# Kernel tuning notes

Hardware: AMD Instinct MI355X
Metric: run time of the kernel (lower is better)

The kernel has to match this reference:

```python
import jax, jax.numpy as jnp
import numpy as np

# Static problem dims (match input_specs / init_kwargs)
B, NQ, C, H = 2, 900, 256, 8
HGT, WID = 64, 64            # single-scale feature map (input_spatial_shapes = [[64, 64]])
N = HGT * WID                # 4096 keys
DH = C // H                  # head dim 32
RPE_HID = 512
STRIDE = 16                  # feature_stride


def setup_inputs() -> dict:
    key = jax.random.key(0)
    ks = jax.random.split(key, 24)
    p = lambda k, shape: jax.random.normal(k, shape, jnp.float32) * 0.02
    # reference boxes (cx, cy, w, h) in pixel coords of a 1024x1024 image
    ref = jax.random.uniform(ks[0], (B, NQ, 1, 4), jnp.float32)
    ref = jnp.concatenate([ref[..., :2] * (WID * STRIDE), ref[..., 2:] * 128.0], axis=-1)
    return {
        "vggt_features": jnp.zeros((1,), jnp.float32),  # unused by forward (kept for signature fidelity)
        "query": jax.random.normal(ks[1], (B, NQ, C), jnp.float32),
        "reference_2d": ref,
        "k_input_flatten": jax.random.normal(ks[2], (B, N, C), jnp.float32),
        "v_input_flatten": jax.random.normal(ks[3], (B, N, C), jnp.float32),
        "input_spatial_shapes": jnp.array([[HGT, WID]], jnp.int32),
        "input_padding_mask": jnp.zeros((B, N), jnp.bool_),
        # cpb_mlp1 (x) and cpb_mlp2 (y): Linear(2,512)+ReLU+Linear(512,H,no bias); stored as [in,out]
        "W1x": p(ks[4], (2, RPE_HID)), "b1x": jnp.zeros((RPE_HID,), jnp.float32), "W2x": p(ks[5], (RPE_HID, H)),
        "W1y": p(ks[6], (2, RPE_HID)), "b1y": jnp.zeros((RPE_HID,), jnp.float32), "W2y": p(ks[7], (RPE_HID, H)),
        "Wq": p(ks[8], (C, C)), "bq": jnp.zeros((C,), jnp.float32),
        "Wk": p(ks[9], (C, C)), "bk": jnp.zeros((C,), jnp.float32),
        "Wv": p(ks[10], (C, C)), "bv": jnp.zeros((C,), jnp.float32),
        "Wp": p(ks[11], (C, C)), "bp": jnp.zeros((C,), jnp.float32),
    }


def _mlp(d, W1, b1, W2):
    return jax.nn.relu(d @ W1 + b1) @ W2


def reference(vggt_features, query, reference_2d, k_input_flatten, v_input_flatten,
              input_spatial_shapes, input_padding_mask,
              W1x, b1x, W2x, W1y, b1y, W2y, Wq, bq, Wk, bk, Wv, bv, Wp, bp):
    h, w = HGT, WID  # static (input_spatial_shapes[0] == [HGT, WID])
    scale = DH ** -0.5
    # cxcywh -> xyxy: [B, NQ, 1, 4]
    xyxy = jnp.concatenate([reference_2d[..., :2] - reference_2d[..., 2:] / 2,
                            reference_2d[..., :2] + reference_2d[..., 2:] / 2], axis=-1)
    # pixel-center grid coords (linspace(0.5, w-0.5, w) * stride)
    pos_x = ((jnp.arange(w, dtype=jnp.float32) + 0.5) * STRIDE)[None, None, :, None]
    pos_y = ((jnp.arange(h, dtype=jnp.float32) + 0.5) * STRIDE)[None, None, :, None]
    delta_x = xyxy[..., 0::2] - pos_x  # [B, NQ, w, 2]  (x1, x2 rel. to columns)
    delta_y = xyxy[..., 1::2] - pos_y  # [B, NQ, h, 2]  (y1, y2 rel. to rows)
    rpe_x = _mlp(delta_x, W1x, b1x, W2x)  # [B, NQ, w, H]
    rpe_y = _mlp(delta_y, W1y, b1y, W2y)  # [B, NQ, h, H]
    # broadcast add over (row, col) then flatten spatial -> [B, H, NQ, N]
    rpe = (rpe_x[:, :, None] + rpe_y[:, :, :, None]).reshape(B, NQ, h * w, H).transpose(0, 3, 1, 2)
    q = (query @ Wq + bq).reshape(B, NQ, H, DH).transpose(0, 2, 1, 3) * scale  # [B,H,NQ,DH]
    k = (k_input_flatten @ Wk + bk).reshape(B, N, H, DH).transpose(0, 2, 1, 3)  # [B,H,N,DH]
    v = (v_input_flatten @ Wv + bv).reshape(B, N, H, DH).transpose(0, 2, 1, 3)  # [B,H,N,DH]
    attn = jnp.einsum('bhqd,bhkd->bhqk', q, k) + rpe
    attn = attn + input_padding_mask[:, None, None, :].astype(attn.dtype) * (-100.0)
    # torch.clip_ to finfo(min,max) is an identity on finite values; softmax follows
    attn = jax.nn.softmax(attn, axis=-1)
    x = jnp.einsum('bhqk,bhkd->bhqd', attn, v).transpose(0, 2, 1, 3).reshape(B, NQ, C)
    return x @ Wp + bp
```

## Files before the change

kernel.cpp:

```cpp
#include <hip/hip_runtime.h>
#include <hip/hip_bf16.h>
#include <cmath>

#define B_ 2
#define NQ_ 900
#define N_ 4096
#define LOG2E 1.4426950408889634f

typedef __attribute__((ext_vector_type(4))) float f32x4;
typedef __attribute__((ext_vector_type(8))) short s16x8;
typedef __attribute__((ext_vector_type(8))) _Float16 f16x8;

__device__ inline short f2bf(float x) {
    union { __hip_bfloat16 b; short s; } u;
    u.b = __float2bfloat16(x);
    return u.s;
}
__device__ inline short f2h(float x) {
    _Float16 h = (_Float16)x;
    return __builtin_bit_cast(short, h);
}

template <int CTRL>
__device__ inline float dppf(float x) {
    int xi = __builtin_bit_cast(int, x);
    int r = __builtin_amdgcn_update_dpp(xi, xi, CTRL, 0xF, 0xF, true);
    return __builtin_bit_cast(float, r);
}
__device__ inline float rowmax16(float v) {
    v = fmaxf(v, dppf<0x121>(v));
    v = fmaxf(v, dppf<0x122>(v));
    v = fmaxf(v, dppf<0x124>(v));
    v = fmaxf(v, dppf<0x128>(v));
    return v;
}
__device__ inline float rowsum16(float v) {
    v += dppf<0x121>(v);
    v += dppf<0x122>(v);
    v += dppf<0x124>(v);
    v += dppf<0x128>(v);
    return v;
}

__global__ __launch_bounds__(256) void proj_kernel(
    const float* __restrict__ query, const float* __restrict__ kin,
    const float* __restrict__ vin,
    const float* __restrict__ Wq, const float* __restrict__ Wk,
    const float* __restrict__ Wv,
    const float* __restrict__ bqv, const float* __restrict__ bkv,
    const float* __restrict__ bvv,
    unsigned short* __restrict__ qbf, unsigned short* __restrict__ kbf,
    unsigned short* __restrict__ vbf, float qscale)
{
    const int mtx = blockIdx.z;
    const float* X = mtx == 0 ? query : mtx == 1 ? kin : vin;
    const float* W = mtx == 0 ? Wq : mtx == 1 ? Wk : Wv;
    const float* bias = mtx == 0 ? bqv : mtx == 1 ? bkv : bvv;
    unsigned short* Y = mtx == 0 ? qbf : mtx == 1 ? kbf : vbf;
    const int M = mtx == 0 ? 1800 : 8192;
    const int m0 = blockIdx.x * 64;
    if (m0 >= M) return;
    const float alpha = mtx == 0 ? qscale : 1.0f;
    const int rows_per_b = mtx == 0 ? 900 : 4096;
    const int ROWS = mtx == 0 ? 960 : 4096;

    __shared__ short Ab[16384];
    __shared__ short Bb[16384];
    const int tid = threadIdx.x;
    const int w = tid >> 6, l = tid & 63, quad = l >> 4, l15 = l & 15;
    const int wq = tid & 3, mm = tid >> 2;

    {
        const bool valid = (m0 + mm) < M;
        const float* xr = X + (size_t)(m0 + mm) * 256;
        #pragma unroll
        for (int it = 0; it < 8; ++it) {
            int g2 = it * 4 + wq;
            float4 a0 = make_float4(0.f, 0.f, 0.f, 0.f), a1 = a0;
            if (valid) {
                a0 = *(const float4*)(xr + g2 * 8);
                a1 = *(const float4*)(xr + g2 * 8 + 4);
            }
            uint4 pk;
            pk.x = (unsigned)(unsigned short)f2bf(a0.x) | ((unsigned)(unsigned short)f2bf(a0.y) << 16);
            pk.y = (unsigned)(unsigned short)f2bf(a0.z) | ((unsigned)(unsigned short)f2bf(a0.w) << 16);
            pk.z = (unsigned)(unsigned short)f2bf(a1.x) | ((unsigned)(unsigned short)f2bf(a1.y) << 16);
            pk.w = (unsigned)(unsigned short)f2bf(a1.z) | ((unsigned)(unsigned short)f2bf(a1.w) << 16);
            *(uint4*)(Ab + (it * 256 + mm * 4 + wq) * 8) = pk;
        }
    }

    for (int nt0 = 0; nt0 < 4; ++nt0) {
        const int n0 = nt0 * 64;
        {
            const float* wcol = W + n0 + mm;
            #pragma unroll
            for (int it = 0; it < 8; ++it) {
                int g2 = it * 4 + wq;
                uint4 wk4;
                wk4.x = (unsigned)(unsigned short)f2bf(wcol[(g2 * 8 + 0) * 256])
                      | ((unsigned)(unsigned short)f2bf(wcol[(g2 * 8 + 1) * 256]) << 16);
                wk4.y = (unsigned)(unsigned short)f2bf(wcol[(g2 * 8 + 2) * 256])
                      | ((unsigned)(unsigned short)f2bf(wcol[(g2 * 8 + 3) * 256]) << 16);
                wk4.z = (unsigned)(unsigned short)f2bf(wcol[(g2 * 8 + 4) * 256])
                      | ((unsigned)(unsigned short)f2bf(wcol[(g2 * 8 + 5) * 256]) << 16);
                wk4.w = (unsigned)(unsigned short)f2bf(wcol[(g2 * 8 + 6) * 256])
                      | ((unsigned)(unsigned short)f2bf(wcol[(g2 * 8 + 7) * 256]) << 16);
                *(uint4*)(Bb + (it * 256 + mm * 4 + wq) * 8) = wk4;
            }
        }
        __syncthreads();

        f32x4 acc[4] = {{0.f,0.f,0.f,0.f},{0.f,0.f,0.f,0.f},{0.f,0.f,0.f,0.f},{0.f,0.f,0.f,0.f}};
        #pragma unroll
        for (int kc = 0; kc < 8; ++kc) {
            s16x8 a = *(const s16x8*)(Ab + (kc * 256 + (w * 16 + l15) * 4 + quad) * 8);
            #pragma unroll
            for (int nt = 0; nt < 4; ++nt) {
                s16x8 bf = *(const s16x8*)(Bb + (kc * 256 + (nt * 16 + l15) * 4 + quad) * 8);
                acc[nt] = __builtin_amdgcn_mfma_f32_16x16x32_bf16(a, bf, acc[nt], 0, 0, 0);
            }
        }
        __syncthreads();

        #pragma unroll
        for (int nt = 0; nt < 4; ++nt) {
            int n = n0 + nt * 16 + l15;
            float bs = bias[n];
            int h = n >> 5, d = n & 31;
            #pragma unroll
            for (int r = 0; r < 4; ++r) {
                int row = m0 + w * 16 + quad * 4 + r;
                if (row < M) {
                    int b = row / rows_per_b;
                    int pos = row - b * rows_per_b;
                    Y[((size_t)(b * 8 + h) * ROWS + pos) * 32 + d] =
                        (unsigned short)f2bf((acc[nt][r] + bs) * alpha);
                }
            }
        }
    }
}

__global__ __launch_bounds__(256) void outproj_kernel(
    const float* __restrict__ X, const float* __restrict__ W,
    const float* __restrict__ bias, float* __restrict__ Y, int M)
{
    __shared__ short Abh[4096], Abl[4096], Bbh[4096], Bbl[4096];
    const int tid = threadIdx.x;
    const int m0 = blockIdx.x * 64, n0 = blockIdx.y * 64;
    const int w = tid >> 6, l = tid & 63, quad = l >> 4, l15 = l & 15;
    const int wq = tid & 3, mm = tid >> 2;
    const bool valid = (m0 + mm) < M;
    const float* xr = X + (size_t)(m0 + mm) * 256;
    const float* wcol = W + n0 + mm;

    f32x4 acc[4] = {{0.f,0.f,0.f,0.f},{0.f,0.f,0.f,0.f},{0.f,0.f,0.f,0.f},{0.f,0.f,0.f,0.f}};

    for (int kq = 0; kq < 4; ++kq) {
        #pragma unroll
        for (int it = 0; it < 2; ++it) {
            int g2 = it * 4 + wq;
            int kbase = kq * 64 + g2 * 8;
            float av[8], bv[8];
            #pragma unroll
            for (int j = 0; j < 8; ++j) {
                av[j] = valid ? xr[kbase + j] : 0.f;
                bv[j] = wcol[(kbase + j) * 256];
            }
            uint4 ah, al, bh, bl;
            unsigned* ahp = (unsigned*)&ah; unsigned* alp = (unsigned*)&al;
            unsigned* bhp = (unsigned*)&bh; unsigned* blp = (unsigned*)&bl;
            #pragma unroll
            for (int j2 = 0; j2 < 4; ++j2) {
                _Float16 h0 = (_Float16)av[j2 * 2], h1 = (_Float16)av[j2 * 2 + 1];
                ahp[j2] = (unsigned)(unsigned short)__builtin_bit_cast(short, h0)
                        | ((unsigned)(unsigned short)__builtin_bit_cast(short, h1) << 16);
                alp[j2] = (unsigned)(unsigned short)f2h(av[j2 * 2] - (float)h0)
                        | ((unsigned)(unsigned short)f2h(av[j2 * 2 + 1] - (float)h1) << 16);
                _Float16 g0 = (_Float16)bv[j2 * 2], g1 = (_Float16)bv[j2 * 2 + 1];
                bhp[j2] = (unsigned)(unsigned short)__builtin_bit_cast(short, g0)
                        | ((unsigned)(unsigned short)__builtin_bit_cast(short, g1) << 16);
                blp[j2] = (unsigned)(unsigned short)f2h(bv[j2 * 2] - (float)g0)
                        | ((unsigned)(unsigned short)f2h(bv[j2 * 2 + 1] - (float)g1) << 16);
            }
            int gi = (it * 256 + mm * 4 + wq) * 8;
            *(uint4*)(Abh + gi) = ah;
            *(uint4*)(Abl + gi) = al;
            *(uint4*)(Bbh + gi) = bh;
            *(uint4*)(Bbl + gi) = bl;
        }
        __syncthreads();

        #pragma unroll
        for (int kc = 0; kc < 2; ++kc) {
            int ga = (kc * 256 + (w * 16 + l15) * 4 + quad) * 8;
            f16x8 ah = *(const f16x8*)(Abh + ga);
            f16x8 al = *(const f16x8*)(Abl + ga);
            #pragma unroll
            for (int nt = 0; nt < 4; ++nt) {
                int gb = (kc * 256 + (nt * 16 + l15) * 4 + quad) * 8;
                f16x8 bh = *(const f16x8*)(Bbh + gb);
                f16x8 bl = *(const f16x8*)(Bbl + gb);
                acc[nt] = __builtin_amdgcn_mfma_f32_16x16x32_f16(ah, bh, acc[nt], 0, 0, 0);
                acc[nt] = __builtin_amdgcn_mfma_f32_16x16x32_f16(ah, bl, acc[nt], 0, 0, 0);
                acc[nt] = __builtin_amdgcn_mfma_f32_16x16x32_f16(al, bh, acc[nt], 0, 0, 0);
            }
        }
        __syncthreads();
    }

    #pragma unroll
    for (int nt = 0; nt < 4; ++nt) {
        int n = n0 + nt * 16 + l15;
        float bs = bias[n];
        #pragma unroll
        for (int r = 0; r < 4; ++r) {
            int row = m0 + w * 16 + quad * 4 + r;
            if (row < M)
                Y[(size_t)row * 256 + n] = acc[nt][r] + bs;
        }
    }
}

__global__ __launch_bounds__(512) void rpe3_kernel(
    const float* __restrict__ ref2d,
    const float* __restrict__ W1x, const float* __restrict__ b1x,
    const float* __restrict__ W1y, const float* __restrict__ b1y,
    const float* __restrict__ W2x, const float* __restrict__ W2y,
    float* __restrict__ rpe_x, float* __restrict__ rpe_y)
{
    __shared__ short sw2h[8192], sw2l[8192];
    __shared__ float4 sUV[2 * 576];

    const int tid = threadIdx.x;
    for (int i = tid; i < 8192; i += 512) {
        int g = i >> 3, j = i & 7;
        int kcg = g >> 6, rr = g & 63, n = rr >> 2, q4 = rr & 3;
        int k = kcg * 32 + q4 * 8 + j;
        float val = ((n < 8) ? W2x[k * 8 + n] : W2y[k * 8 + (n - 8)]) * LOG2E;
        _Float16 hi = (_Float16)val;
        sw2h[i] = __builtin_bit_cast(short, hi);
        sw2l[i] = f2h(val - (float)hi);
    }
    {
        int k = tid;
        float w1x0 = W1x[k], w1x1 = W1x[512 + k];
        float w1y0 = W1y[k], w1y1 = W1y[512 + k];
        float bx = b1x[k], by = b1y[k];
        float vx = -(w1x0 + w1x1), vy = -(w1y0 + w1y1);
        #pragma unroll
        for (int q2 = 0; q2 < 2; ++q2) {
            const float4 bb = *(const float4*)(ref2d + (size_t)(blockIdx.x * 2 + q2) * 4);
            float ux = fmaf(w1x0, bb.x - bb.z * 0.5f, fmaf(w1x1, bb.x + bb.z * 0.5f, bx));
            float uy = fmaf(w1y0, bb.y - bb.w * 0.5f, fmaf(w1y1, bb.y + bb.w * 0.5f, by));
            sUV[q2 * 576 + (k >> 3) * 9 + (k & 7)] = make_float4(ux, vx, uy, vy);
        }
    }

    const int w = tid >> 6, l = tid & 63, quad = l >> 4, l15 = l & 15;
    const int qi = w >> 2, wrow = w & 3;
    const int bq = blockIdx.x * 2 + qi;
    const int row = wrow * 16 + l15;
    const float pc = (row + 0.5f) * 16.0f;

    __syncthreads();

    f32x4 accx = {0.f, 0.f, 0.f, 0.f}, accy = {0.f, 0.f, 0.f, 0.f};
    for (int kc = 0; kc < 16; ++kc) {
        f16x8 axh, axl, ayh, ayl;
        #pragma unroll
        for (int i = 0; i < 8; ++i) {
            float4 u = sUV[qi * 576 + (kc * 4 + quad) * 9 + i];
            float hx = fmaxf(fmaf(u.y, pc, u.x), 0.f);
            float hy = fmaxf(fmaf(u.w, pc, u.z), 0.f);
            _Float16 xh = (_Float16)hx;
            _Float16 yh = (_Float16)hy;
            axh[i] = xh;
            axl[i] = (_Float16)(hx - (float)xh);
            ayh[i] = yh;
            ayl[i] = (_Float16)(hy - (float)yh);
        }
        f16x8 bh = *(const f16x8*)(sw2h + (kc * 64 + l15 * 4 + quad) * 8);
        f16x8 bl = *(const f16x8*)(sw2l + (kc * 64 + l15 * 4 + quad) * 8);
        accx = __builtin_amdgcn_mfma_f32_16x16x32_f16(axh, bh, accx, 0, 0, 0);
        accx = __builtin_amdgcn_mfma_f32_16x16x32_f16(axh, bl, accx, 0, 0, 0);
        accx = __builtin_amdgcn_mfma_f32_16x16x32_f16(axl, bh, accx, 0, 0, 0);
        accy = __builtin_amdgcn_mfma_f32_16x16x32_f16(ayh, bh, accy, 0, 0, 0);
        accy = __builtin_amdgcn_mfma_f32_16x16x32_f16(ayh, bl, accy, 0, 0, 0);
        accy = __builtin_amdgcn_mfma_f32_16x16x32_f16(ayl, bh, accy, 0, 0, 0);
    }

    #pragma unroll
    for (int rr = 0; rr < 4; ++rr) {
        int row_out = wrow * 16 + quad * 4 + rr;
        if (l15 < 8) rpe_x[((size_t)l15 * 1800 + bq) * 64 + row_out] = accx[rr];
        else         rpe_y[((size_t)(l15 - 8) * 1800 + bq) * 64 + row_out] = accy[rr];
    }
}

__global__ __launch_bounds__(512, 4) void attn_mfma_kernel(
    const unsigned short* __restrict__ qb16, const unsigned short* __restrict__ kb16,
    const unsigned short* __restrict__ vb16,
    const float* __restrict__ rpe_x, const float* __restrict__ rpe_y,
    const unsigned char* __restrict__ mask, float* __restrict__ part)
{
    __shared__ short skf[4 * 2048];
    __shared__ short svt[4 * 2048];
    __shared__ short spb[8 * 544];
    __shared__ float sry[32 * 33];
    __shared__ unsigned long long smaskb[32];
    __shared__ float sm[8][16], sl[8][16], sMf[32], sLf[32];

    const int tid = threadIdx.x;
    const int qb = blockIdx.x, b = blockIdx.z;
    const int h = blockIdx.y & 7, kv = blockIdx.y >> 3;
    const int q0 = qb * 32;
    const int w = tid >> 6, l = tid & 63;
    const int qsub = w >> 3 ? 0 : 0;
    const int qs = w >> 2, g = w & 3;
    const int quad = l >> 4, l15 = l & 15;

    const unsigned short* qg = qb16 + (size_t)(b * 8 + h) * 960 * 32;
    const unsigned short* kg = kb16 + (size_t)(b * 8 + h) * 4096 * 32 + (size_t)kv * 2048 * 32;
    const unsigned short* vg = vb16 + (size_t)(b * 8 + h) * 4096 * 32 + (size_t)kv * 2048 * 32;
    const float* rxh = rpe_x + ((size_t)h * 1800 + b * NQ_) * 64;
    const float* ryh = rpe_y + ((size_t)h * 1800 + b * NQ_) * 64;

    for (int i = tid; i < 1024; i += 512) {
        int qq = q0 + (i >> 5), p = i & 31;
        float vy = 0.f;
        if (qq < NQ_)
            vy = ryh[(size_t)qq * 64 + kv * 32 + p];
        sry[(i >> 5) * 33 + p] = vy;
    }
    #pragma unroll
    for (int j = 0; j < 4; ++j) {
        int c = w * 4 + j;
        unsigned long long bits = __ballot(mask[(size_t)b * N_ + (kv * 32 + c) * 64 + l] != 0);
        if (l == 0) smaskb[c] = bits;
    }

    s16x8 qa = *(const s16x8*)(qg + (size_t)(q0 + qs * 16 + l15) * 32 + quad * 8);

    f32x4 rx4[4];
    #pragma unroll
    for (int t = 0; t < 4; ++t)
        #pragma unroll
        for (int r = 0; r < 4; ++r) {
            int qq = q0 + qs * 16 + quad * 4 + r;
            rx4[t][r] = (qq < NQ_) ? rxh[(size_t)qq * 64 + t * 16 + l15] : 0.f;
        }

    const int sg = tid >> 7, role = (tid >> 6) & 1, stl = tid & 63;
    int eoff[4];
    if (role == 0) {
        #pragma unroll
        for (int t = 0; t < 4; ++t)
            eoff[t] = (t * 16 + (stl & 15)) * 32 + (stl >> 4) * 8;
    } else {
        #pragma unroll
        for (int t = 0; t < 4; ++t)
            eoff[t] = stl * 32 + t * 8;
    }
    const unsigned short* src = role ? vg : kg;

    uint4 pf[4];
    {
        size_t cb = (size_t)(sg * 8) * 2048;
        #pragma unroll
        for (int t = 0; t < 4; ++t) pf[t] = *(const uint4*)(src + cb + eoff[t]);
    }

    float mrow[4] = {-INFINITY, -INFINITY, -INFINITY, -INFINITY};
    float lrow[4] = {0.f, 0.f, 0.f, 0.f};
    f32x4 acc0 = {0.f, 0.f, 0.f, 0.f}, acc1 = {0.f, 0.f, 0.f, 0.f};
    short* pw = spb + w * 544;

    for (int i = 0; i < 8; ++i) {
        __syncthreads();
        if (role == 0) {
            #pragma unroll
            for (int t = 0; t < 4; ++t)
                *(uint4*)(skf + sg * 2048 + (t * 64 + stl) * 8) = pf[t];
        } else {
            short* vtw = svt + sg * 2048;
            #pragma unroll
            for (int t = 0; t < 4; ++t) {
                const unsigned short* pv = (const unsigned short*)&pf[t];
                #pragma unroll
                for (int j = 0; j < 8; ++j) {
                    int d = t * 8 + j;
                    vtw[d * 64 + (((stl >> 3) ^ (d & 7)) << 3) + (stl & 7)] = (short)pv[j];
                }
            }
        }
        __syncthreads();

        {
            int inext = (i + 1 < 8) ? i + 1 : 7;
            size_t cb = (size_t)(sg * 8 + inext) * 2048;
            #pragma unroll
            for (int t = 0; t < 4; ++t) pf[t] = *(const uint4*)(src + cb + eoff[t]);
        }

        const int lc = g * 8 + i;
        const short* kf = skf + g * 2048;

        f32x4 sc[4];
        #pragma unroll
        for (int t = 0; t < 4; ++t) {
            s16x8 kb = *(const s16x8*)(kf + (t * 64 + l) * 8);
            sc[t] = __builtin_amdgcn_mfma_f32_16x16x32_bf16(qa, kb, rx4[t], 0, 0, 0);
        }
        float ryv[4];
        #pragma unroll
        for (int r = 0; r < 4; ++r)
            ryv[r] = sry[(qs * 16 + quad * 4 + r) * 33 + lc];
        unsigned long long mb = smaskb[lc];
        if (mb) {
            #pragma unroll
            for (int t = 0; t < 4; ++t) {
                float mk = ((mb >> (t * 16 + l15)) & 1ULL) ? -144.2695f : 0.f;
                #pragma unroll
                for (int r = 0; r < 4; ++r) sc[t][r] += mk;
            }
        }

        float cmr[4];
        #pragma unroll
        for (int r = 0; r < 4; ++r)
            cmr[r] = fmaxf(fmaxf(sc[0][r], sc[1][r]), fmaxf(sc[2][r], sc[3][r])) + ryv[r];

        int ok = (cmr[0] <= mrow[0] + 8.f) & (cmr[1] <= mrow[1] + 8.f)
               & (cmr[2] <= mrow[2] + 8.f) & (cmr[3] <= mrow[3] + 8.f);
        if (!__all(ok)) {
            #pragma unroll
            for (int r = 0; r < 4; ++r) {
                float cm = rowmax16(cmr[r]);
                float mnew = fmaxf(mrow[r], cm);
                float al = exp2f(mrow[r] - mnew);
                mrow[r] = mnew;
                lrow[r] *= al;
                acc0[r] *= al;
                acc1[r] *= al;
            }
        }

        float msub[4];
        #pragma unroll
        for (int r = 0; r < 4; ++r) msub[r] = mrow[r] - ryv[r];
        #pragma unroll
        for (int t = 0; t < 4; ++t)
            #pragma unroll
            for (int r = 0; r < 4; ++r)
                sc[t][r] = exp2f(sc[t][r] - msub[r]);
        #pragma unroll
        for (int r = 0; r < 4; ++r)
            lrow[r] += (sc[0][r] + sc[1][r]) + (sc[2][r] + sc[3][r]);

        const short* vt = svt + g * 2048;
        #pragma unroll
        for (int hh = 0; hh < 2; ++hh) {
            #pragma unroll
            for (int tt = 0; tt < 2; ++tt) {
                int t = hh * 2 + tt;
                int gphys = (tt * 2 + (l15 >> 3)) ^ quad;
                #pragma unroll
                for (int r = 0; r < 4; ++r)
                    pw[(gphys * 17 + quad * 4 + r) * 8 + (l15 & 7)] = f2bf(sc[t][r]);
            }
            int gph_r = quad ^ (l15 >> 2);
            s16x8 pa  = *(const s16x8*)(pw + (gph_r * 17 + l15) * 8);
            int ksw = ((hh * 4 + quad) ^ (l15 & 7)) * 8;
            s16x8 vb0 = *(const s16x8*)(vt + l15 * 64 + ksw);
            s16x8 vb1 = *(const s16x8*)(vt + (16 + l15) * 64 + ksw);
            acc0 = __builtin_amdgcn_mfma_f32_16x16x32_bf16(pa, vb0, acc0, 0, 0, 0);
            acc1 = __builtin_amdgcn_mfma_f32_16x16x32_bf16(pa, vb1, acc1, 0, 0, 0);
        }
    }

    #pragma unroll
    for (int r = 0; r < 4; ++r) lrow[r] = rowsum16(lrow[r]);

    __syncthreads();
    if (l15 == 0) {
        #pragma unroll
        for (int r = 0; r < 4; ++r) {
            sm[w][quad * 4 + r] = mrow[r];
            sl[w][quad * 4 + r] = lrow[r];
        }
    }
    __syncthreads();
    float wgt[4], L4[4], M4[4];
    #pragma unroll
    for (int r = 0; r < 4; ++r) {
        int qrow = quad * 4 + r;
        float mm = -INFINITY;
        #pragma unroll
        for (int gg = 0; gg < 4; ++gg) mm = fmaxf(mm, sm[qs * 4 + gg][qrow]);
        float LL = 0.f;
        #pragma unroll
        for (int gg = 0; gg < 4; ++gg)
            LL += exp2f(sm[qs * 4 + gg][qrow] - mm) * sl[qs * 4 + gg][qrow];
        wgt[r] = exp2f(mrow[r] - mm);
        L4[r] = LL;
        M4[r] = mm;
    }
    if (g == 0 && l15 == 0) {
        #pragma unroll
        for (int r = 0; r < 4; ++r) {
            sLf[qs * 16 + quad * 4 + r] = L4[r];
            sMf[qs * 16 + quad * 4 + r] = M4[r];
        }
    }

    float* obuf = (float*)skf;
    for (int gg = 0; gg < 4; ++gg) {
        if (g == gg) {
            #pragma unroll
            for (int r = 0; r < 4; ++r) {
                int idx = (qs * 16 + quad * 4 + r) * 33 + l15;
                float v0 = wgt[r] * acc0[r];
                float v1 = wgt[r] * acc1[r];
                if (gg == 0) { obuf[idx] = v0; obuf[idx + 16] = v1; }
                else         { obuf[idx] += v0; obuf[idx + 16] += v1; }
            }
        }
        __syncthreads();
    }

    float* po = part + (size_t)(((b * 8 + h) * 29 + qb) * 2 + kv) * 1088;
    for (int i = tid; i < 1024; i += 512)
        po[i] = obuf[(i >> 5) * 33 + (i & 31)];
    if (tid < 32) {
        po[1024 + tid] = sMf[tid];
        po[1056 + tid] = sLf[tid];
    }
}

__global__ __launch_bounds__(256) void attn_merge_kernel(
    const float* __restrict__ part, float* __restrict__ xout)
{
    const int qb = blockIdx.x, h = blockIdx.y, b = blockIdx.z;
    const float* p0 = part + (size_t)(((b * 8 + h) * 29 + qb) * 2) * 1088;
    const float* p1 = p0 + 1088;
    __shared__ float a0s[32], a1s[32], iLs[32];
    const int tid = threadIdx.x;
    if (tid < 32) {
        float m0 = p0[1024 + tid], m1 = p1[1024 + tid];
        float M = fmaxf(m0, m1);
        float a0 = exp2f(m0 - M), a1 = exp2f(m1 - M);
        float L = a0 * p0[1056 + tid] + a1 * p1[1056 + tid];
        a0s[tid] = a0; a1s[tid] = a1; iLs[tid] = 1.0f / L;
    }
    __syncthreads();
    int i = tid * 4;
    int ql = i >> 5, d = i & 31;
    int qq = qb * 32 + ql;
    if (qq < NQ_) {
        const f32x4 v0 = *(const f32x4*)(p0 + i);
        const f32x4 v1 = *(const f32x4*)(p1 + i);
        float a0 = a0s[ql], a1 = a1s[ql], iL = iLs[ql];
        f32x4 o;
        #pragma unroll
        for (int j = 0; j < 4; ++j)
            o[j] = (a0 * v0[j] + a1 * v1[j]) * iL;
        *(f32x4*)(&xout[(size_t)(b * NQ_ + qq) * 256 + h * 32 + d]) = o;
    }
}

extern "C" void kernel_launch(void* const* d_in, const int* in_sizes, int n_in,
                              void* d_out, int out_size, void* d_ws, size_t ws_size,
                              hipStream_t stream)
{
    const float* query = (const float*)d_in[1];
    const float* ref2d = (const float*)d_in[2];
    const float* kin   = (const float*)d_in[3];
    const float* vin   = (const float*)d_in[4];
    const unsigned char* mask = (const unsigned char*)d_in[6];
    const float* W1x = (const float*)d_in[7];
    const float* b1x = (const float*)d_in[8];
    const float* W2x = (const float*)d_in[9];
    const float* W1y = (const float*)d_in[10];
    const float* b1y = (const float*)d_in[11];
    const float* W2y = (const float*)d_in[12];
    const float* Wq  = (const float*)d_in[13];
    const float* bq  = (const float*)d_in[14];
    const float* Wk  = (const float*)d_in[15];
    const float* bk  = (const float*)d_in[16];
    const float* Wv  = (const float*)d_in[17];
    const float* bv  = (const float*)d_in[18];
    const float* Wp  = (const float*)d_in[19];
    const float* bp  = (const float*)d_in[20];

    char* wsb = (char*)d_ws;
    unsigned short* qbf = (unsigned short*)(wsb);
    unsigned short* kbf = (unsigned short*)(wsb +   983040);
    unsigned short* vbf = (unsigned short*)(wsb +  5177344);
    float* rxws = (float*)(wsb +  9371648);
    float* ryws = (float*)(wsb + 13058048);
    float* xws  = (float*)(wsb + 16744448);
    float* part = (float*)(wsb + 18587648);
    float* out  = (float*)d_out;

    const float qscale = LOG2E / sqrtf(32.0f);

    proj_kernel<<<dim3(128, 1, 3), 256, 0, stream>>>(
        query, kin, vin, Wq, Wk, Wv, bq, bk, bv, qbf, kbf, vbf, qscale);
    rpe3_kernel<<<900, 512, 0, stream>>>(
        ref2d, W1x, b1x, W1y, b1y, W2x, W2y, rxws, ryws);
    attn_mfma_kernel<<<dim3(29, 16, B_), 512, 0, stream>>>(
        qbf, kbf, vbf, rxws, ryws, mask, part);
    attn_merge_kernel<<<dim3(29, 8, B_), 256, 0, stream>>>(part, xws);
    outproj_kernel<<<dim3(29, 4), 256, 0, stream>>>(xws, Wp, bp, out, 1800);
}
```

Measured before the change: 235.0 us.

## Transpose QK MFMA so P stays in registers and feeds PV directly

Swaps the MFMA operand order for QK^T so each lane holds one query row's scores, which makes the row max and row sum lane-local (only cross-quad shuffles are needed) and removes the per-row DPP reductions. The P matrix is converted with packed fp16 and fed straight into 16x16x16 f16 MFMAs from registers, removing the shared-memory round trip through spb. V is now stored as fp16 to match. The launch-bounds occupancy hint rises to 8, which puts pressure on register allocation. The change also trades bf16 for fp16 precision on P and V.

```diff
diff --git a/kernel.cpp b/kernel.cpp
--- a/kernel.cpp
+++ b/kernel.cpp
@@ -10,6 +10,8 @@
 typedef __attribute__((ext_vector_type(4))) float f32x4;
 typedef __attribute__((ext_vector_type(8))) short s16x8;
 typedef __attribute__((ext_vector_type(8))) _Float16 f16x8;
+typedef __attribute__((ext_vector_type(4))) __fp16 h16x4;
+typedef __attribute__((ext_vector_type(2))) __fp16 h16x2;
 
 __device__ inline short f2bf(float x) {
     union { __hip_bfloat16 b; short s; } u;
@@ -19,27 +21,6 @@
 __device__ inline short f2h(float x) {
     _Float16 h = (_Float16)x;
     return __builtin_bit_cast(short, h);
-}
-
-template <int CTRL>
-__device__ inline float dppf(float x) {
-    int xi = __builtin_bit_cast(int, x);
-    int r = __builtin_amdgcn_update_dpp(xi, xi, CTRL, 0xF, 0xF, true);
-    return __builtin_bit_cast(float, r);
-}
-__device__ inline float rowmax16(float v) {
-    v = fmaxf(v, dppf<0x121>(v));
-    v = fmaxf(v, dppf<0x122>(v));
-    v = fmaxf(v, dppf<0x124>(v));
-    v = fmaxf(v, dppf<0x128>(v));
-    return v;
-}
-__device__ inline float rowsum16(float v) {
-    v += dppf<0x121>(v);
-    v += dppf<0x122>(v);
-    v += dppf<0x124>(v);
-    v += dppf<0x128>(v);
-    return v;
 }
 
 __global__ __launch_bounds__(256) void proj_kernel(
@@ -134,8 +115,9 @@
                 if (row < M) {
                     int b = row / rows_per_b;
                     int pos = row - b * rows_per_b;
+                    float v = (acc[nt][r] + bs) * alpha;
                     Y[((size_t)(b * 8 + h) * ROWS + pos) * 32 + d] =
-                        (unsigned short)f2bf((acc[nt][r] + bs) * alpha);
+                        (unsigned short)(mtx == 2 ? f2h(v) : f2bf(v));
                 }
             }
         }
@@ -299,7 +281,7 @@
     }
 }
 
-__global__ __launch_bounds__(512, 4) void attn_mfma_kernel(
+__global__ __launch_bounds__(512, 8) void attn_mfma_kernel(
     const unsigned short* __restrict__ qb16, const unsigned short* __restrict__ kb16,
     const unsigned short* __restrict__ vb16,
     const float* __restrict__ rpe_x, const float* __restrict__ rpe_y,
@@ -307,7 +289,6 @@
 {
     __shared__ short skf[4 * 2048];
     __shared__ short svt[4 * 2048];
-    __shared__ short spb[8 * 544];
     __shared__ float sry[32 * 33];
     __shared__ unsigned long long smaskb[32];
     __shared__ float sm[8][16], sl[8][16], sMf[32], sLf[32];
@@ -317,7 +298,6 @@
     const int h = blockIdx.y & 7, kv = blockIdx.y >> 3;
     const int q0 = qb * 32;
     const int w = tid >> 6, l = tid & 63;
-    const int qsub = w >> 3 ? 0 : 0;
     const int qs = w >> 2, g = w & 3;
     const int quad = l >> 4, l15 = l & 15;
 
@@ -328,11 +308,10 @@
     const float* ryh = rpe_y + ((size_t)h * 1800 + b * NQ_) * 64;
 
     for (int i = tid; i < 1024; i += 512) {
-        int qq = q0 + (i >> 5), p = i & 31;
-        float vy = 0.f;
-        if (qq < NQ_)
-            vy = ryh[(size_t)qq * 64 + kv * 32 + p];
-        sry[(i >> 5) * 33 + p] = vy;
+        int p = i & 31, ql = i >> 5;
+        int qq = q0 + ql;
+        float vy = (qq < NQ_) ? ryh[(size_t)qq * 64 + kv * 32 + p] : 0.f;
+        sry[p * 33 + ql] = vy;
     }
     #pragma unroll
     for (int j = 0; j < 4; ++j) {
@@ -343,14 +322,13 @@
 
     s16x8 qa = *(const s16x8*)(qg + (size_t)(q0 + qs * 16 + l15) * 32 + quad * 8);
 
+    const int qq_l = q0 + qs * 16 + l15;
     f32x4 rx4[4];
     #pragma unroll
     for (int t = 0; t < 4; ++t)
         #pragma unroll
-        for (int r = 0; r < 4; ++r) {
-            int qq = q0 + qs * 16 + quad * 4 + r;
-            rx4[t][r] = (qq < NQ_) ? rxh[(size_t)qq * 64 + t * 16 + l15] : 0.f;
-        }
+        for (int r = 0; r < 4; ++r)
+            rx4[t][r] = (qq_l < NQ_) ? rxh[(size_t)qq_l * 64 + t * 16 + quad * 4 + r] : 0.f;
 
     const int sg = tid >> 7, role = (tid >> 6) & 1, stl = tid & 63;
     int eoff[4];
@@ -372,10 +350,9 @@
         for (int t = 0; t < 4; ++t) pf[t] = *(const uint4*)(src + cb + eoff[t]);
     }
 
-    float mrow[4] = {-INFINITY, -INFINITY, -INFINITY, -INFINITY};
-    float lrow[4] = {0.f, 0.f, 0.f, 0.f};
+    float mrow = -INFINITY;
+    float lrow = 0.f;
     f32x4 acc0 = {0.f, 0.f, 0.f, 0.f}, acc1 = {0.f, 0.f, 0.f, 0.f};
-    short* pw = spb + w * 544;
 
     for (int i = 0; i < 8; ++i) {
         __syncthreads();
@@ -411,108 +388,83 @@
         #pragma unroll
         for (int t = 0; t < 4; ++t) {
             s16x8 kb = *(const s16x8*)(kf + (t * 64 + l) * 8);
-            sc[t] = __builtin_amdgcn_mfma_f32_16x16x32_bf16(qa, kb, rx4[t], 0, 0, 0);
-        }
-        float ryv[4];
-        #pragma unroll
-        for (int r = 0; r < 4; ++r)
-            ryv[r] = sry[(qs * 16 + quad * 4 + r) * 33 + lc];
+            sc[t] = __builtin_amdgcn_mfma_f32_16x16x32_bf16(kb, qa, rx4[t], 0, 0, 0);
+        }
+        float ryv = sry[lc * 33 + qs * 16 + l15];
         unsigned long long mb = smaskb[lc];
         if (mb) {
-            #pragma unroll
-            for (int t = 0; t < 4; ++t) {
-                float mk = ((mb >> (t * 16 + l15)) & 1ULL) ? -144.2695f : 0.f;
-                #pragma unroll
-                for (int r = 0; r < 4; ++r) sc[t][r] += mk;
-            }
-        }
-
-        float cmr[4];
-        #pragma unroll
-        for (int r = 0; r < 4; ++r)
-            cmr[r] = fmaxf(fmaxf(sc[0][r], sc[1][r]), fmaxf(sc[2][r], sc[3][r])) + ryv[r];
-
-        int ok = (cmr[0] <= mrow[0] + 8.f) & (cmr[1] <= mrow[1] + 8.f)
-               & (cmr[2] <= mrow[2] + 8.f) & (cmr[3] <= mrow[3] + 8.f);
-        if (!__all(ok)) {
-            #pragma unroll
-            for (int r = 0; r < 4; ++r) {
-                float cm = rowmax16(cmr[r]);
-                float mnew = fmaxf(mrow[r], cm);
-                float al = exp2f(mrow[r] - mnew);
-                mrow[r] = mnew;
-                lrow[r] *= al;
-                acc0[r] *= al;
-                acc1[r] *= al;
-            }
-        }
-
-        float msub[4];
-        #pragma unroll
-        for (int r = 0; r < 4; ++r) msub[r] = mrow[r] - ryv[r];
-        #pragma unroll
-        for (int t = 0; t < 4; ++t)
-            #pragma unroll
-            for (int r = 0; r < 4; ++r)
-                sc[t][r] = exp2f(sc[t][r] - msub[r]);
-        #pragma unroll
-        for (int r = 0; r < 4; ++r)
-            lrow[r] += (sc[0][r] + sc[1][r]) + (sc[2][r] + sc[3][r]);
-
-        const short* vt = svt + g * 2048;
-        #pragma unroll
-        for (int hh = 0; hh < 2; ++hh) {
-            #pragma unroll
-            for (int tt = 0; tt < 2; ++tt) {
-                int t = hh * 2 + tt;
-                int gphys = (tt * 2 + (l15 >> 3)) ^ quad;
+            unsigned long long mq = mb >> (quad * 4);
+            #pragma unroll
+            for (int t = 0; t < 4; ++t)
                 #pragma unroll
                 for (int r = 0; r < 4; ++r)
-                    pw[(gphys * 17 + quad * 4 + r) * 8 + (l15 & 7)] = f2bf(sc[t][r]);
-            }
-            int gph_r = quad ^ (l15 >> 2);
-            s16x8 pa  = *(const s16x8*)(pw + (gph_r * 17 + l15) * 8);
-            int ksw = ((hh * 4 + quad) ^ (l15 & 7)) * 8;
-            s16x8 vb0 = *(const s16x8*)(vt + l15 * 64 + ksw);
-            s16x8 vb1 = *(const s16x8*)(vt + (16 + l15) * 64 + ksw);
-            acc0 = __builtin_amdgcn_mfma_f32_16x16x32_bf16(pa, vb0, acc0, 0, 0, 0);
-            acc1 = __builtin_amdgcn_mfma_f32_16x16x32_bf16(pa, vb1, acc1, 0, 0, 0);
-        }
-    }
-
+                    sc[t][r] += ((mq >> (t * 16 + r)) & 1ULL) ? -144.2695f : 0.f;
+        }
+
+        float cmx = fmaxf(fmaxf(fmaxf(sc[0][0], sc[0][1]), fmaxf(sc[0][2], sc[0][3])),
+                          fmaxf(fmaxf(sc[1][0], sc[1][1]), fmaxf(sc[1][2], sc[1][3])));
+        cmx = fmaxf(cmx, fmaxf(fmaxf(fmaxf(sc[2][0], sc[2][1]), fmaxf(sc[2][2], sc[2][3])),
+                               fmaxf(fmaxf(sc[3][0], sc[3][1]), fmaxf(sc[3][2], sc[3][3]))));
+        cmx += ryv;
+
+        if (!__all(cmx <= mrow + 8.f)) {
+            float cm = cmx;
+            cm = fmaxf(cm, __shfl_xor(cm, 16));
+            cm = fmaxf(cm, __shfl_xor(cm, 32));
+            float mnew = fmaxf(mrow, cm);
+            float al = exp2f(mrow - mnew);
+            mrow = mnew;
+            lrow *= al;
+            #pragma unroll
+            for (int r = 0; r < 4; ++r) { acc0[r] *= al; acc1[r] *= al; }
+        }
+
+        float msub = mrow - ryv;
+        #pragma unroll
+        for (int t = 0; t < 4; ++t)
+            #pragma unroll
+            for (int r = 0; r < 4; ++r)
+                sc[t][r] = exp2f(sc[t][r] - msub);
+        lrow += ((sc[0][0] + sc[0][1]) + (sc[0][2] + sc[0][3]))
+              + ((sc[1][0] + sc[1][1]) + (sc[1][2] + sc[1][3]))
+              + ((sc[2][0] + sc[2][1]) + (sc[2][2] + sc[2][3]))
+              + ((sc[3][0] + sc[3][1]) + (sc[3][2] + sc[3][3]));
+
+        const short* vt = svt + g * 2048;
+        #pragma unroll
+        for (int t = 0; t < 4; ++t) {
+            h16x2 p01 = __builtin_amdgcn_cvt_pkrtz(sc[t][0], sc[t][1]);
+            h16x2 p23 = __builtin_amdgcn_cvt_pkrtz(sc[t][2], sc[t][3]);
+            h16x4 pa;
+            pa[0] = p01[0]; pa[1] = p01[1]; pa[2] = p23[0]; pa[3] = p23[1];
+            int pbase = (((t * 2 + (quad >> 1)) ^ (l15 & 7)) << 3) + ((quad & 1) << 2);
+            h16x4 v0 = *(const h16x4*)(vt + l15 * 64 + pbase);
+            h16x4 v1 = *(const h16x4*)(vt + (16 + l15) * 64 + pbase);
+            acc0 = __builtin_amdgcn_mfma_f32_16x16x16f16(v0, pa, acc0, 0, 0, 0);
+            acc1 = __builtin_amdgcn_mfma_f32_16x16x16f16(v1, pa, acc1, 0, 0, 0);
+        }
+    }
+
+    lrow += __shfl_xor(lrow, 16);
+    lrow += __shfl_xor(lrow, 32);
+
+    __syncthreads();
+    if (quad == 0) {
+        sm[w][l15] = mrow;
+        sl[w][l15] = lrow;
+    }
+    __syncthreads();
+    float mm = -INFINITY;
     #pragma unroll
-    for (int r = 0; r < 4; ++r) lrow[r] = rowsum16(lrow[r]);
-
-    __syncthreads();
-    if (l15 == 0) {
-        #pragma unroll
-        for (int r = 0; r < 4; ++r) {
-            sm[w][quad * 4 + r] = mrow[r];
-            sl[w][quad * 4 + r] = lrow[r];
-        }
-    }
-    __syncthreads();
-    float wgt[4], L4[4], M4[4];
+    for (int gg = 0; gg < 4; ++gg) mm = fmaxf(mm, sm[qs * 4 + gg][l15]);
+    float LL = 0.f;
     #pragma unroll
-    for (int r = 0; r < 4; ++r) {
-        int qrow = quad * 4 + r;
-        float mm = -INFINITY;
-        #pragma unroll
-        for (int gg = 0; gg < 4; ++gg) mm = fmaxf(mm, sm[qs * 4 + gg][qrow]);
-        float LL = 0.f;
-        #pragma unroll
-        for (int gg = 0; gg < 4; ++gg)
-            LL += exp2f(sm[qs * 4 + gg][qrow] - mm) * sl[qs * 4 + gg][qrow];
-        wgt[r] = exp2f(mrow[r] - mm);
-        L4[r] = LL;
-        M4[r] = mm;
-    }
-    if (g == 0 && l15 == 0) {
-        #pragma unroll
-        for (int r = 0; r < 4; ++r) {
-            sLf[qs * 16 + quad * 4 + r] = L4[r];
-            sMf[qs * 16 + quad * 4 + r] = M4[r];
-        }
+    for (int gg = 0; gg < 4; ++gg)
+        LL += exp2f(sm[qs * 4 + gg][l15] - mm) * sl[qs * 4 + gg][l15];
+    float wgt = exp2f(mrow - mm);
+    if (g == 0 && quad == 0) {
+        sMf[qs * 16 + l15] = mm;
+        sLf[qs * 16 + l15] = LL;
     }
 
     float* obuf = (float*)skf;
@@ -520,9 +472,9 @@
         if (g == gg) {
             #pragma unroll
             for (int r = 0; r < 4; ++r) {
-                int idx = (qs * 16 + quad * 4 + r) * 33 + l15;
-                float v0 = wgt[r] * acc0[r];
-                float v1 = wgt[r] * acc1[r];
+                int idx = (qs * 16 + l15) * 33 + quad * 4 + r;
+                float v0 = wgt * acc0[r];
+                float v1 = wgt * acc1[r];
                 if (gg == 0) { obuf[idx] = v0; obuf[idx + 16] = v1; }
                 else         { obuf[idx] += v0; obuf[idx + 16] += v1; }
             }
```

New measurement: 423.5 us. 80.2% more time.
